# Kernel tuning notes

Measured on AMD Instinct MI355X. Metric: run time of the kernel, lower is better.

## Reference

```python
import jax, jax.numpy as jnp
import numpy as np

B = 16384          # batch_size
NF = 50            # n_fields
K = 16             # embedding_dim
V = 1_000_000      # input_dim (vocab)
H = 400            # fc hidden
NNZ = B * NF


def _xavier(key, shape):
    fan_in, fan_out = shape
    lim = (6.0 / (fan_in + fan_out)) ** 0.5
    return jax.random.uniform(key, shape, minval=-lim, maxval=lim, dtype=jnp.float32)


def setup_inputs() -> dict:
    key = jax.random.key(0)
    ks = jax.random.split(key, 12)
    feats = jax.random.randint(ks[0], (NNZ,), 0, V)
    # n_fields contiguous features per sample (required by view(batch_size,-1))
    index = jnp.repeat(jnp.arange(B), NF)
    values = jax.random.uniform(ks[1], (NNZ,), dtype=jnp.float32)
    bias = jnp.zeros((1, 1), jnp.float32)
    weights = _xavier(ks[2], (V, 1))
    embedding = _xavier(ks[3], (V, K))
    d = NF * K  # 800
    W0 = _xavier(ks[4], (d, H))
    b0 = jax.random.normal(ks[5], (1, 1), jnp.float32)
    W1 = _xavier(ks[6], (H, H))
    b1 = jax.random.normal(ks[7], (1, 1), jnp.float32)
    W2 = _xavier(ks[8], (H, 1))
    b2 = jax.random.normal(ks[9], (1, 1), jnp.float32)
    return dict(index=index, feats=feats, values=values, bias=bias,
                weights=weights, embedding=embedding,
                W0=W0, b0=b0, W1=W1, b1=b1, W2=W2, b2=b2, batch_size=B)


def reference(index, feats, values, bias, weights, embedding,
              W0, b0, W1, b1, W2, b2, batch_size):
    # gather (F.embedding)
    w = weights[feats, 0]              # [nnz]
    emb = embedding[feats]             # [nnz, K]

    # first order: segment-sum of w*v, plus bias ([B] + [1,1] -> [1,B], as in torch)
    first = jax.ops.segment_sum(w * values, index, num_segments=batch_size) + bias

    # second order: FM pooling trick, fused over all K dims in one segment reduce
    ev = emb * values[:, None]                                        # [nnz, K]
    s1 = jax.ops.segment_sum(ev, index, num_segments=batch_size)      # [B, K]
    s2 = jax.ops.segment_sum(ev * ev, index, num_segments=batch_size) # [B, K]
    second = 0.5 * jnp.sum(s1 * s1 - s2, axis=1)                      # [B]

    # higher order MLP (relu on every layer, scalar biases)
    x = emb.reshape(batch_size, -1)    # [B, NF*K]
    x = jax.nn.relu(x @ W0 + b0)
    x = jax.nn.relu(x @ W1 + b1)
    x = jax.nn.relu(x @ W2 + b2)       # [B, 1]
    higher = x.reshape(-1)             # [B]

    return jax.nn.sigmoid(first + second + higher)  # [1, B]
```

## Files before the change

### kernel.cpp

```cpp
#include <hip/hip_runtime.h>
#include <hip/hip_bf16.h>


#define BATCH 16384
#define NFLD  50
#define EK    16
#define DDIM  800
#define HDIM  400
#define HPAD  416
#define NPAD  512

#define TB_W0 400
#define TB_W1 208
#define TBLK  (TB_W0 + TB_W1)
#define GBLK  (BATCH / 16)

#define MROWS 64
#define NCOLS 448
#define P1    (DDIM / 32)
#define P2    (HPAD / 32)
#define H0S   424

#define PH1B(b) ((b) * 32768)
#define PH2B(b) ((b) * 28672)
#define H0OFF   98304
#define REDOFF  152576
#define LDSSZ   154624

#define VMCNT(N) asm volatile("s_waitcnt vmcnt(" #N ")" ::: "memory")

typedef __attribute__((ext_vector_type(8))) __bf16 bf16x8;
typedef __attribute__((ext_vector_type(4))) float  f32x4;

typedef const __attribute__((address_space(1))) unsigned int* gas_u32p;
typedef __attribute__((address_space(3))) unsigned int*       las_u32p;

__device__ __forceinline__ void gld_lds16(const void* g, void* l) {
    __builtin_amdgcn_global_load_lds((gas_u32p)g, (las_u32p)l, 16, 0, 0);
}

__device__ __forceinline__ void bar() {
    __builtin_amdgcn_sched_barrier(0);
    __builtin_amdgcn_s_barrier();
    __builtin_amdgcn_sched_barrier(0);
}

__global__ __launch_bounds__(256) void prep_kernel(
    const float* __restrict__ W0, const float* __restrict__ W1,
    __hip_bfloat16* __restrict__ W0t, __hip_bfloat16* __restrict__ W1t,
    const int* __restrict__ feats, const float* __restrict__ values,
    const float* __restrict__ biasp, const float* __restrict__ weights,
    const float* __restrict__ embedding,
    float* __restrict__ fs, __hip_bfloat16* __restrict__ x)
{
    const int bid = blockIdx.x;
    if (bid < TBLK) {
        const int which = bid >= TB_W0;
        const int i  = which ? bid - TB_W0 : bid;
        const int nx = which ? 13 : 25;
        const int bx = i % nx, by = i / nx;
        const float* src = which ? W1 : W0;
        __hip_bfloat16* dst = which ? W1t : W0t;
        const int srcK = which ? HDIM : DDIM;
        const int dstCols = which ? HPAD : DDIM;

        __shared__ float tile[32][33];
        const int tx = threadIdx.x & 31, ty = threadIdx.x >> 5;
        const int k0 = bx * 32, n0 = by * 32;
#pragma unroll
        for (int r = 0; r < 4; ++r) {
            int k = k0 + ty + r * 8;
            int n = n0 + tx;
            float v = (k < srcK && n < HDIM) ? src[(long)k * HDIM + n] : 0.f;
            tile[ty + r * 8][tx] = v;
        }
        __syncthreads();
#pragma unroll
        for (int r = 0; r < 4; ++r) {
            int n = n0 + ty + r * 8;
            int k = k0 + tx;
            if (k < dstCols)
                dst[(long)n * dstCols + k] = __float2bfloat16(tile[tx][ty + r * 8]);
        }
        return;
    }

    const int wave = threadIdx.x >> 6;
    const int lane = threadIdx.x & 63;
    const int r    = lane >> 2, c = lane & 3;
    const int sbase = (bid - TBLK) * 16 + wave * 4;

    int   f[4] = {0, 0, 0, 0};
    float v[4] = {0.f, 0.f, 0.f, 0.f};
    float wsum[4] = {0.f, 0.f, 0.f, 0.f};
#pragma unroll
    for (int q = 0; q < 4; ++q) {
        const long base = (long)(sbase + q) * NFLD;
        if (lane < NFLD) {
            f[q] = feats[base + lane];
            v[q] = values[base + lane];
            wsum[q] = weights[f[q]] * v[q];
        }
    }

    int   fj[4][4]; float vj[4][4];
#pragma unroll
    for (int q = 0; q < 4; ++q)
#pragma unroll
        for (int p = 0; p < 4; ++p) {
            const int j = p * 16 + r;
            if (p < 3 || r < 2) {
                fj[q][p] = __shfl(f[q], j);
                vj[q][p] = __shfl(v[q], j);
            }
        }
    float4 e[4][4];
#pragma unroll
    for (int q = 0; q < 4; ++q)
#pragma unroll
        for (int p = 0; p < 4; ++p)
            if (p < 3 || r < 2)
                e[q][p] = *(const float4*)(embedding + (long)fj[q][p] * EK + c * 4);

#pragma unroll
    for (int q = 0; q < 4; ++q) {
        const int s = sbase + q;
        f32x4 s1 = {0.f, 0.f, 0.f, 0.f}, s2 = {0.f, 0.f, 0.f, 0.f};
#pragma unroll
        for (int p = 0; p < 4; ++p) {
            const int j = p * 16 + r;
            if (p < 3 || r < 2) {
                f32x4 ef = {e[q][p].x, e[q][p].y, e[q][p].z, e[q][p].w};
                f32x4 ev = ef * vj[q][p];
                s1 += ev;
                s2 += ev * ev;
                __hip_bfloat16 pk[4] = {
                    __float2bfloat16(e[q][p].x), __float2bfloat16(e[q][p].y),
                    __float2bfloat16(e[q][p].z), __float2bfloat16(e[q][p].w)};
                *(uint2*)&x[(long)s * DDIM + j * EK + c * 4] = *(uint2*)pk;
            }
        }
#pragma unroll
        for (int m = 4; m <= 32; m <<= 1) {
            s1.x += __shfl_xor(s1.x, m); s1.y += __shfl_xor(s1.y, m);
            s1.z += __shfl_xor(s1.z, m); s1.w += __shfl_xor(s1.w, m);
            s2.x += __shfl_xor(s2.x, m); s2.y += __shfl_xor(s2.y, m);
            s2.z += __shfl_xor(s2.z, m); s2.w += __shfl_xor(s2.w, m);
        }
        float t = (s1.x * s1.x - s2.x) + (s1.y * s1.y - s2.y)
                + (s1.z * s1.z - s2.z) + (s1.w * s1.w - s2.w);
        t += __shfl_xor(t, 1); t += __shfl_xor(t, 2);
        float w = wsum[q];
        w += __shfl_xor(w, 1);  w += __shfl_xor(w, 2);
        w += __shfl_xor(w, 4);  w += __shfl_xor(w, 8);
        w += __shfl_xor(w, 16); w += __shfl_xor(w, 32);
        if (lane == 0) fs[s] = w + 0.5f * t + biasp[0];
    }
}

__global__ __launch_bounds__(448) void fused_mlp_kernel(
    const __hip_bfloat16* __restrict__ x,
    const __hip_bfloat16* __restrict__ W0t, const __hip_bfloat16* __restrict__ W1t,
    const float* __restrict__ b0p, const float* __restrict__ b1p,
    const float* __restrict__ W2, const float* __restrict__ b2p,
    const float* __restrict__ fs, float* __restrict__ out)
{
    __shared__ __align__(16) char lds[LDSSZ];
    __hip_bfloat16* h0p = (__hip_bfloat16*)(lds + H0OFF);
    float*          red = (float*)(lds + REDOFF);

    const int tid  = threadIdx.x;
    const int wave = tid >> 6, lane = tid & 63;
    const int l16  = lane & 15, quad = lane >> 4;
    const int m0 = blockIdx.x * MROWS;
    const int nbase = wave * 64;

    const int rl  = lane >> 2;
    const int swc = ((lane & 3) ^ ((lane >> 3) & 3)) * 8;
    const int qsw = (quad ^ ((l16 >> 1) & 3)) * 8;

    const float b0 = b0p[0];
    const float b1 = b1p[0];

    const int sstart = (wave < 4) ? wave * 5 : 20 + (wave - 4) * 4;
    const int scnt   = (wave < 4) ? 5 : 4;
    auto stage1 = [&](int p, int b) {
        const int k0 = p * 32;
        char* dst = lds + PH1B(b);
#pragma unroll
        for (int c = 0; c < 5; ++c) {
            if (c < scnt) {
                const int id = sstart + c;
                const __hip_bfloat16* src = (id < 4)
                    ? x   + (long)(m0 + id * 16 + rl) * DDIM + k0 + swc
                    : W0t + (long)((id - 4) * 16 + rl) * DDIM + k0 + swc;
                gld_lds16(src, dst + id * 1024 + lane * 16);
            }
        }
    };

    f32x4 acc[4][4] = {};
    auto compute1 = [&](int b) {
        const __hip_bfloat16* s = (const __hip_bfloat16*)(lds + PH1B(b));
        bf16x8 af[4], bfr[4];
#pragma unroll
        for (int i = 0; i < 4; ++i)
            af[i] = *(const bf16x8*)&s[i * 512 + l16 * 32 + qsw];
#pragma unroll
        for (int j = 0; j < 4; ++j)
            bfr[j] = *(const bf16x8*)&s[(4 + wave * 4 + j) * 512 + l16 * 32 + qsw];
        __builtin_amdgcn_s_setprio(1);
#pragma unroll
        for (int i = 0; i < 4; ++i)
#pragma unroll
            for (int j = 0; j < 4; ++j)
                acc[i][j] = __builtin_amdgcn_mfma_f32_16x16x32_bf16(
                    af[i], bfr[j], acc[i][j], 0, 0, 0);
        __builtin_amdgcn_s_setprio(0);
    };

    stage1(0, 0);
    stage1(1, 1);
    for (int p = 0; p < P1; ++p) {
        if (p + 1 < P1) { VMCNT(4); } else { VMCNT(0); }
        bar();
        if (p + 2 < P1) stage1(p + 2, (p + 2) % 3);
        compute1(p % 3);
    }
    bar();

    auto stage2 = [&](int p, int b) {
        const int k0 = p * 32;
#pragma unroll
        for (int c = 0; c < 4; ++c) {
            const int ch = wave * 4 + c;
            gld_lds16(W1t + (long)(ch * 16 + rl) * HPAD + k0 + swc,
                      lds + PH2B(b) + ch * 1024 + lane * 16);
        }
    };
    stage2(0, 0);
    stage2(1, 1);

#pragma unroll
    for (int i = 0; i < 4; ++i)
#pragma unroll
        for (int j = 0; j < 4; ++j) {
            const int col = nbase + j * 16 + l16;
            if (col < HPAD) {
#pragma unroll
                for (int r = 0; r < 4; ++r) {
                    const int row = i * 16 + quad * 4 + r;
                    float v = acc[i][j][r] + b0;
                    v = v > 0.f ? v : 0.f;
                    if (col >= HDIM) v = 0.f;
                    h0p[row * H0S + col] = __float2bfloat16(v);
                }
            }
        }

    f32x4 acc2[4][4] = {};
    float w2v[4];
#pragma unroll
    for (int j = 0; j < 4; ++j) {
        const int col = nbase + j * 16 + l16;
        w2v[j] = (col < HDIM) ? W2[col] : 0.f;
    }
    auto compute2 = [&](int p, int b) {
        const __hip_bfloat16* s = (const __hip_bfloat16*)(lds + PH2B(b));
        bf16x8 af[4], bfr[4];
#pragma unroll
        for (int i = 0; i < 4; ++i)
            af[i] = *(const bf16x8*)&h0p[(i * 16 + l16) * H0S + p * 32 + quad * 8];
#pragma unroll
        for (int j = 0; j < 4; ++j)
            bfr[j] = *(const bf16x8*)&s[(wave * 4 + j) * 512 + l16 * 32 + qsw];
        __builtin_amdgcn_s_setprio(1);
#pragma unroll
        for (int i = 0; i < 4; ++i)
#pragma unroll
            for (int j = 0; j < 4; ++j)
                acc2[i][j] = __builtin_amdgcn_mfma_f32_16x16x32_bf16(
                    af[i], bfr[j], acc2[i][j], 0, 0, 0);
        __builtin_amdgcn_s_setprio(0);
    };

    asm volatile("s_waitcnt lgkmcnt(0)" ::: "memory");
    bar();

    for (int p = 0; p < P2; ++p) {
        if (p + 1 < P2) { VMCNT(4); } else { VMCNT(0); }
        bar();
        if (p + 2 < P2) stage2(p + 2, (p + 2) % 3);
        compute2(p, p % 3);
    }

    if (tid < MROWS) red[tid * 8 + 7] = 0.f;
#pragma unroll
    for (int i = 0; i < 4; ++i)
#pragma unroll
        for (int r = 0; r < 4; ++r) {
            float ps = 0.f;
#pragma unroll
            for (int j = 0; j < 4; ++j) {
                float v = acc2[i][j][r] + b1;
                v = v > 0.f ? v : 0.f;
                ps += v * w2v[j];
            }
            ps += __shfl_xor(ps, 1); ps += __shfl_xor(ps, 2);
            ps += __shfl_xor(ps, 4); ps += __shfl_xor(ps, 8);
            if (l16 == 0)
                red[(i * 16 + quad * 4 + r) * 8 + wave] = ps;
        }
    __syncthreads();

    if (tid < MROWS) {
        const float4 r0 = *(const float4*)&red[tid * 8];
        const float4 r1 = *(const float4*)&red[tid * 8 + 4];
        const float s = ((r0.x + r0.y) + (r0.z + r0.w))
                      + ((r1.x + r1.y) + (r1.z + r1.w));
        float hv = s + b2p[0];
        hv = hv > 0.f ? hv : 0.f;
        const float z = fs[m0 + tid] + hv;
        out[m0 + tid] = 1.f / (1.f + __expf(-z));
    }
}

extern "C" void kernel_launch(void* const* d_in, const int* in_sizes, int n_in,
                              void* d_out, int out_size, void* d_ws, size_t ws_size,
                              hipStream_t stream)
{
    const int*   feats     = (const int*)d_in[1];
    const float* values    = (const float*)d_in[2];
    const float* bias      = (const float*)d_in[3];
    const float* weights   = (const float*)d_in[4];
    const float* embedding = (const float*)d_in[5];
    const float* W0 = (const float*)d_in[6];
    const float* b0 = (const float*)d_in[7];
    const float* W1 = (const float*)d_in[8];
    const float* b1 = (const float*)d_in[9];
    const float* W2 = (const float*)d_in[10];
    const float* b2 = (const float*)d_in[11];

    char* ws = (char*)d_ws;
    size_t off = 0;
    auto alloc = [&](size_t bytes) {
        void* p = ws + off;
        off += (bytes + 255) & ~(size_t)255;
        return p;
    };
    float*          fs   = (float*)alloc((size_t)BATCH * 4);
    __hip_bfloat16* x    = (__hip_bfloat16*)alloc((size_t)BATCH * DDIM * 2);
    __hip_bfloat16* W0t  = (__hip_bfloat16*)alloc((size_t)NPAD * DDIM * 2);
    __hip_bfloat16* W1t  = (__hip_bfloat16*)alloc((size_t)NPAD * HPAD * 2);
    (void)ws_size; (void)in_sizes; (void)n_in; (void)out_size;

    prep_kernel<<<dim3(TBLK + GBLK), 256, 0, stream>>>(
        W0, W1, W0t, W1t, feats, values, bias, weights, embedding, fs, x);
    fused_mlp_kernel<<<dim3(BATCH / MROWS), 448, 0, stream>>>(
        x, W0t, W1t, b0, b1, W2, b2, fs, (float*)d_out);
}
```

Baseline: 167.5 us.

## Fuse embedding gather and FM pooling into the MLP kernel via LDS

The embedding gather, first/second-order FM sums and bf16 packing of the activation panel move from the prep kernel into the fused MLP kernel. Each block gathers its 64 rows directly into a swizzled LDS panel, so the bf16 x matrix and the fs vector no longer round-trip through global memory. The block grows to 512 threads with only 7 waves doing MFMA, and W0/W1 staging drops from triple to double buffering with full vmcnt(0) waits. The risks are a serialized gather latency at kernel start and less load/compute overlap in the GEMM loops.

Measured after the change: 173.0 us. +3.3%, slower.

```diff
diff --git a/kernel.cpp b/kernel.cpp
--- a/kernel.cpp
+++ b/kernel.cpp
@@ -13,19 +13,17 @@
 #define TB_W0 400
 #define TB_W1 208
 #define TBLK  (TB_W0 + TB_W1)
-#define GBLK  (BATCH / 16)
 
 #define MROWS 64
-#define NCOLS 448
 #define P1    (DDIM / 32)
 #define P2    (HPAD / 32)
 #define H0S   424
 
-#define PH1B(b) ((b) * 32768)
-#define PH2B(b) ((b) * 28672)
-#define H0OFF   98304
-#define REDOFF  152576
-#define LDSSZ   154624
+#define BOFF   102400
+#define BBUF   28672
+#define REDOFF (BOFF + 2 * BBUF)
+#define FSLOFF (REDOFF + 2048)
+#define LDSSZ  (FSLOFF + 256)
 
 #define VMCNT(N) asm volatile("s_waitcnt vmcnt(" #N ")" ::: "memory")
 
@@ -47,168 +45,141 @@
 
 __global__ __launch_bounds__(256) void prep_kernel(
     const float* __restrict__ W0, const float* __restrict__ W1,
-    __hip_bfloat16* __restrict__ W0t, __hip_bfloat16* __restrict__ W1t,
+    __hip_bfloat16* __restrict__ W0t, __hip_bfloat16* __restrict__ W1t)
+{
+    const int bid = blockIdx.x;
+    const int which = bid >= TB_W0;
+    const int i  = which ? bid - TB_W0 : bid;
+    const int nx = which ? 13 : 25;
+    const int bx = i % nx, by = i / nx;
+    const float* src = which ? W1 : W0;
+    __hip_bfloat16* dst = which ? W1t : W0t;
+    const int srcK = which ? HDIM : DDIM;
+    const int dstCols = which ? HPAD : DDIM;
+
+    __shared__ float tile[32][33];
+    const int tx = threadIdx.x & 31, ty = threadIdx.x >> 5;
+    const int k0 = bx * 32, n0 = by * 32;
+#pragma unroll
+    for (int r = 0; r < 4; ++r) {
+        int k = k0 + ty + r * 8;
+        int n = n0 + tx;
+        float v = (k < srcK && n < HDIM) ? src[(long)k * HDIM + n] : 0.f;
+        tile[ty + r * 8][tx] = v;
+    }
+    __syncthreads();
+#pragma unroll
+    for (int r = 0; r < 4; ++r) {
+        int n = n0 + ty + r * 8;
+        int k = k0 + tx;
+        if (k < dstCols)
+            dst[(long)n * dstCols + k] = __float2bfloat16(tile[tx][ty + r * 8]);
+    }
+}
+
+__global__ __launch_bounds__(512, 2) void fused_mlp_kernel(
     const int* __restrict__ feats, const float* __restrict__ values,
     const float* __restrict__ biasp, const float* __restrict__ weights,
     const float* __restrict__ embedding,
-    float* __restrict__ fs, __hip_bfloat16* __restrict__ x)
-{
-    const int bid = blockIdx.x;
-    if (bid < TBLK) {
-        const int which = bid >= TB_W0;
-        const int i  = which ? bid - TB_W0 : bid;
-        const int nx = which ? 13 : 25;
-        const int bx = i % nx, by = i / nx;
-        const float* src = which ? W1 : W0;
-        __hip_bfloat16* dst = which ? W1t : W0t;
-        const int srcK = which ? HDIM : DDIM;
-        const int dstCols = which ? HPAD : DDIM;
-
-        __shared__ float tile[32][33];
-        const int tx = threadIdx.x & 31, ty = threadIdx.x >> 5;
-        const int k0 = bx * 32, n0 = by * 32;
-#pragma unroll
-        for (int r = 0; r < 4; ++r) {
-            int k = k0 + ty + r * 8;
-            int n = n0 + tx;
-            float v = (k < srcK && n < HDIM) ? src[(long)k * HDIM + n] : 0.f;
-            tile[ty + r * 8][tx] = v;
-        }
-        __syncthreads();
-#pragma unroll
-        for (int r = 0; r < 4; ++r) {
-            int n = n0 + ty + r * 8;
-            int k = k0 + tx;
-            if (k < dstCols)
-                dst[(long)n * dstCols + k] = __float2bfloat16(tile[tx][ty + r * 8]);
-        }
-        return;
-    }
-
-    const int wave = threadIdx.x >> 6;
-    const int lane = threadIdx.x & 63;
-    const int r    = lane >> 2, c = lane & 3;
-    const int sbase = (bid - TBLK) * 16 + wave * 4;
-
-    int   f[4] = {0, 0, 0, 0};
-    float v[4] = {0.f, 0.f, 0.f, 0.f};
-    float wsum[4] = {0.f, 0.f, 0.f, 0.f};
-#pragma unroll
-    for (int q = 0; q < 4; ++q) {
-        const long base = (long)(sbase + q) * NFLD;
-        if (lane < NFLD) {
-            f[q] = feats[base + lane];
-            v[q] = values[base + lane];
-            wsum[q] = weights[f[q]] * v[q];
-        }
-    }
-
-    int   fj[4][4]; float vj[4][4];
-#pragma unroll
-    for (int q = 0; q < 4; ++q)
-#pragma unroll
-        for (int p = 0; p < 4; ++p) {
-            const int j = p * 16 + r;
-            if (p < 3 || r < 2) {
-                fj[q][p] = __shfl(f[q], j);
-                vj[q][p] = __shfl(v[q], j);
-            }
-        }
-    float4 e[4][4];
-#pragma unroll
-    for (int q = 0; q < 4; ++q)
-#pragma unroll
-        for (int p = 0; p < 4; ++p)
-            if (p < 3 || r < 2)
-                e[q][p] = *(const float4*)(embedding + (long)fj[q][p] * EK + c * 4);
-
-#pragma unroll
-    for (int q = 0; q < 4; ++q) {
-        const int s = sbase + q;
-        f32x4 s1 = {0.f, 0.f, 0.f, 0.f}, s2 = {0.f, 0.f, 0.f, 0.f};
-#pragma unroll
-        for (int p = 0; p < 4; ++p) {
-            const int j = p * 16 + r;
-            if (p < 3 || r < 2) {
-                f32x4 ef = {e[q][p].x, e[q][p].y, e[q][p].z, e[q][p].w};
-                f32x4 ev = ef * vj[q][p];
-                s1 += ev;
-                s2 += ev * ev;
-                __hip_bfloat16 pk[4] = {
-                    __float2bfloat16(e[q][p].x), __float2bfloat16(e[q][p].y),
-                    __float2bfloat16(e[q][p].z), __float2bfloat16(e[q][p].w)};
-                *(uint2*)&x[(long)s * DDIM + j * EK + c * 4] = *(uint2*)pk;
-            }
-        }
-#pragma unroll
-        for (int m = 4; m <= 32; m <<= 1) {
-            s1.x += __shfl_xor(s1.x, m); s1.y += __shfl_xor(s1.y, m);
-            s1.z += __shfl_xor(s1.z, m); s1.w += __shfl_xor(s1.w, m);
-            s2.x += __shfl_xor(s2.x, m); s2.y += __shfl_xor(s2.y, m);
-            s2.z += __shfl_xor(s2.z, m); s2.w += __shfl_xor(s2.w, m);
-        }
-        float t = (s1.x * s1.x - s2.x) + (s1.y * s1.y - s2.y)
-                + (s1.z * s1.z - s2.z) + (s1.w * s1.w - s2.w);
-        t += __shfl_xor(t, 1); t += __shfl_xor(t, 2);
-        float w = wsum[q];
-        w += __shfl_xor(w, 1);  w += __shfl_xor(w, 2);
-        w += __shfl_xor(w, 4);  w += __shfl_xor(w, 8);
-        w += __shfl_xor(w, 16); w += __shfl_xor(w, 32);
-        if (lane == 0) fs[s] = w + 0.5f * t + biasp[0];
-    }
-}
-
-__global__ __launch_bounds__(448) void fused_mlp_kernel(
-    const __hip_bfloat16* __restrict__ x,
     const __hip_bfloat16* __restrict__ W0t, const __hip_bfloat16* __restrict__ W1t,
     const float* __restrict__ b0p, const float* __restrict__ b1p,
     const float* __restrict__ W2, const float* __restrict__ b2p,
-    const float* __restrict__ fs, float* __restrict__ out)
+    float* __restrict__ out)
 {
     __shared__ __align__(16) char lds[LDSSZ];
-    __hip_bfloat16* h0p = (__hip_bfloat16*)(lds + H0OFF);
+    __hip_bfloat16* h0p = (__hip_bfloat16*)lds;
     float*          red = (float*)(lds + REDOFF);
+    float*          fsl = (float*)(lds + FSLOFF);
 
     const int tid  = threadIdx.x;
     const int wave = tid >> 6, lane = tid & 63;
     const int l16  = lane & 15, quad = lane >> 4;
     const int m0 = blockIdx.x * MROWS;
-    const int nbase = wave * 64;
 
     const int rl  = lane >> 2;
     const int swc = ((lane & 3) ^ ((lane >> 3) & 3)) * 8;
     const int qsw = (quad ^ ((l16 >> 1) & 3)) * 8;
 
-    const float b0 = b0p[0];
-    const float b1 = b1p[0];
-
-    const int sstart = (wave < 4) ? wave * 5 : 20 + (wave - 4) * 4;
-    const int scnt   = (wave < 4) ? 5 : 4;
-    auto stage1 = [&](int p, int b) {
-        const int k0 = p * 32;
-        char* dst = lds + PH1B(b);
-#pragma unroll
-        for (int c = 0; c < 5; ++c) {
-            if (c < scnt) {
-                const int id = sstart + c;
-                const __hip_bfloat16* src = (id < 4)
-                    ? x   + (long)(m0 + id * 16 + rl) * DDIM + k0 + swc
-                    : W0t + (long)((id - 4) * 16 + rl) * DDIM + k0 + swc;
-                gld_lds16(src, dst + id * 1024 + lane * 16);
+    auto stageB = [&](const __hip_bfloat16* Bt, int ldb, int p, int b) {
+        const int k0  = p * 32;
+        const int nst = (wave < 4) ? 4 : 3;
+        const int st0 = (wave < 4) ? wave * 4 : 16 + (wave - 4) * 3;
+#pragma unroll
+        for (int c = 0; c < 4; ++c) {
+            if (c < nst) {
+                const int ch = st0 + c;
+                gld_lds16(Bt + (long)(ch * 16 + rl) * ldb + k0 + swc,
+                          lds + BOFF + b * BBUF + ch * 1024 + lane * 16);
             }
         }
     };
 
+    stageB(W0t, DDIM, 0, 0);
+
+    {
+        const int s   = tid >> 3;
+        const int sub = tid & 7;
+        const int cq  = sub & 3;
+        const int jh  = sub >> 2;
+        const long sb = (long)(m0 + s) * NFLD;
+        const int pr = s & 15, pg = s >> 4;
+        const int pbase = pg * 1024 + pr * 64 + (cq & 1) * 8;
+        const int sxor  = (pr >> 1) & 3;
+
+        f32x4 s1v = {0.f, 0.f, 0.f, 0.f}, s2v = {0.f, 0.f, 0.f, 0.f};
+        float wsum = 0.f;
+#pragma unroll
+        for (int g = 0; g < 5; ++g) {
+            int ff[5]; float vv[5]; float4 ee[5];
+#pragma unroll
+            for (int k = 0; k < 5; ++k) ff[k] = feats[sb + jh * 25 + g * 5 + k];
+#pragma unroll
+            for (int k = 0; k < 5; ++k) vv[k] = values[sb + jh * 25 + g * 5 + k];
+#pragma unroll
+            for (int k = 0; k < 5; ++k)
+                ee[k] = *(const float4*)(embedding + (long)ff[k] * EK + cq * 4);
+#pragma unroll
+            for (int k = 0; k < 5; ++k) {
+                const int j = jh * 25 + g * 5 + k;
+                f32x4 ef = {ee[k].x, ee[k].y, ee[k].z, ee[k].w};
+                f32x4 ev = ef * vv[k];
+                s1v += ev;
+                s2v += ev * ev;
+                if (cq == 0) wsum += weights[ff[k]] * vv[k];
+                __hip_bfloat16 pk[4] = {
+                    __float2bfloat16(ee[k].x), __float2bfloat16(ee[k].y),
+                    __float2bfloat16(ee[k].z), __float2bfloat16(ee[k].w)};
+                const int slot = (j & 1) * 2 + (cq >> 1);
+                *(uint2*)(lds + (j >> 1) * 4096 + pbase + (slot ^ sxor) * 16) =
+                    *(uint2*)pk;
+            }
+        }
+        s1v.x += __shfl_xor(s1v.x, 4); s1v.y += __shfl_xor(s1v.y, 4);
+        s1v.z += __shfl_xor(s1v.z, 4); s1v.w += __shfl_xor(s1v.w, 4);
+        s2v.x += __shfl_xor(s2v.x, 4); s2v.y += __shfl_xor(s2v.y, 4);
+        s2v.z += __shfl_xor(s2v.z, 4); s2v.w += __shfl_xor(s2v.w, 4);
+        wsum  += __shfl_xor(wsum, 4);
+        float tq = (s1v.x * s1v.x - s2v.x) + (s1v.y * s1v.y - s2v.y)
+                 + (s1v.z * s1v.z - s2v.z) + (s1v.w * s1v.w - s2v.w);
+        tq += __shfl_xor(tq, 1); tq += __shfl_xor(tq, 2);
+        if (sub == 0) fsl[s] = wsum + 0.5f * tq + biasp[0];
+    }
+    asm volatile("s_waitcnt lgkmcnt(0)" ::: "memory");
+
+    const float b0 = b0p[0];
+    const float b1 = b1p[0];
+
     f32x4 acc[4][4] = {};
-    auto compute1 = [&](int b) {
-        const __hip_bfloat16* s = (const __hip_bfloat16*)(lds + PH1B(b));
+    auto compute1 = [&](int p, int b) {
+        const __hip_bfloat16* pan = (const __hip_bfloat16*)lds;
+        const __hip_bfloat16* sB  = (const __hip_bfloat16*)(lds + BOFF + b * BBUF);
         bf16x8 af[4], bfr[4];
 #pragma unroll
         for (int i = 0; i < 4; ++i)
-            af[i] = *(const bf16x8*)&s[i * 512 + l16 * 32 + qsw];
+            af[i] = *(const bf16x8*)&pan[p * 2048 + i * 512 + l16 * 32 + qsw];
 #pragma unroll
         for (int j = 0; j < 4; ++j)
-            bfr[j] = *(const bf16x8*)&s[(4 + wave * 4 + j) * 512 + l16 * 32 + qsw];
+            bfr[j] = *(const bf16x8*)&sB[(wave * 4 + j) * 512 + l16 * 32 + qsw];
         __builtin_amdgcn_s_setprio(1);
 #pragma unroll
         for (int i = 0; i < 4; ++i)
@@ -219,61 +190,47 @@
         __builtin_amdgcn_s_setprio(0);
     };
 
-    stage1(0, 0);
-    stage1(1, 1);
     for (int p = 0; p < P1; ++p) {
-        if (p + 1 < P1) { VMCNT(4); } else { VMCNT(0); }
+        VMCNT(0);
         bar();
-        if (p + 2 < P1) stage1(p + 2, (p + 2) % 3);
-        compute1(p % 3);
+        if (p + 1 < P1) stageB(W0t, DDIM, p + 1, (p + 1) & 1);
+        if (wave < 7) compute1(p, p & 1);
     }
     bar();
 
-    auto stage2 = [&](int p, int b) {
-        const int k0 = p * 32;
-#pragma unroll
-        for (int c = 0; c < 4; ++c) {
-            const int ch = wave * 4 + c;
-            gld_lds16(W1t + (long)(ch * 16 + rl) * HPAD + k0 + swc,
-                      lds + PH2B(b) + ch * 1024 + lane * 16);
-        }
-    };
-    stage2(0, 0);
-    stage2(1, 1);
-
-#pragma unroll
-    for (int i = 0; i < 4; ++i)
-#pragma unroll
-        for (int j = 0; j < 4; ++j) {
-            const int col = nbase + j * 16 + l16;
-            if (col < HPAD) {
-#pragma unroll
-                for (int r = 0; r < 4; ++r) {
-                    const int row = i * 16 + quad * 4 + r;
-                    float v = acc[i][j][r] + b0;
-                    v = v > 0.f ? v : 0.f;
-                    if (col >= HDIM) v = 0.f;
-                    h0p[row * H0S + col] = __float2bfloat16(v);
+    stageB(W1t, HPAD, 0, 0);
+
+    if (wave < 7) {
+#pragma unroll
+        for (int i = 0; i < 4; ++i)
+#pragma unroll
+            for (int j = 0; j < 4; ++j) {
+                const int col = wave * 64 + j * 16 + l16;
+                if (col < HPAD) {
+#pragma unroll
+                    for (int r = 0; r < 4; ++r) {
+                        const int row = i * 16 + quad * 4 + r;
+                        float v = acc[i][j][r] + b0;
+                        v = v > 0.f ? v : 0.f;
+                        if (col >= HDIM) v = 0.f;
+                        h0p[row * H0S + col] = __float2bfloat16(v);
+                    }
                 }
             }
-        }
+    }
+    asm volatile("s_waitcnt lgkmcnt(0)" ::: "memory");
+    bar();
 
     f32x4 acc2[4][4] = {};
-    float w2v[4];
-#pragma unroll
-    for (int j = 0; j < 4; ++j) {
-        const int col = nbase + j * 16 + l16;
-        w2v[j] = (col < HDIM) ? W2[col] : 0.f;
-    }
     auto compute2 = [&](int p, int b) {
-        const __hip_bfloat16* s = (const __hip_bfloat16*)(lds + PH2B(b));
+        const __hip_bfloat16* sB = (const __hip_bfloat16*)(lds + BOFF + b * BBUF);
         bf16x8 af[4], bfr[4];
 #pragma unroll
         for (int i = 0; i < 4; ++i)
             af[i] = *(const bf16x8*)&h0p[(i * 16 + l16) * H0S + p * 32 + quad * 8];
 #pragma unroll
         for (int j = 0; j < 4; ++j)
-            bfr[j] = *(const bf16x8*)&s[(wave * 4 + j) * 512 + l16 * 32 + qsw];
+            bfr[j] = *(const bf16x8*)&sB[(wave * 4 + j) * 512 + l16 * 32 + qsw];
         __builtin_amdgcn_s_setprio(1);
 #pragma unroll
         for (int i = 0; i < 4; ++i)
@@ -284,43 +241,48 @@
         __builtin_amdgcn_s_setprio(0);
     };
 
-    asm volatile("s_waitcnt lgkmcnt(0)" ::: "memory");
-    bar();
-
     for (int p = 0; p < P2; ++p) {
-        if (p + 1 < P2) { VMCNT(4); } else { VMCNT(0); }
+        VMCNT(0);
         bar();
-        if (p + 2 < P2) stage2(p + 2, (p + 2) % 3);
-        compute2(p, p % 3);
+        if (p + 1 < P2) stageB(W1t, HPAD, p + 1, (p + 1) & 1);
+        if (wave < 7) compute2(p, p & 1);
     }
 
     if (tid < MROWS) red[tid * 8 + 7] = 0.f;
-#pragma unroll
-    for (int i = 0; i < 4; ++i)
-#pragma unroll
-        for (int r = 0; r < 4; ++r) {
-            float ps = 0.f;
-#pragma unroll
-            for (int j = 0; j < 4; ++j) {
-                float v = acc2[i][j][r] + b1;
-                v = v > 0.f ? v : 0.f;
-                ps += v * w2v[j];
+    if (wave < 7) {
+        float w2v[4];
+#pragma unroll
+        for (int j = 0; j < 4; ++j) {
+            const int col = wave * 64 + j * 16 + l16;
+            w2v[j] = (col < HDIM) ? W2[col] : 0.f;
+        }
+#pragma unroll
+        for (int i = 0; i < 4; ++i)
+#pragma unroll
+            for (int r = 0; r < 4; ++r) {
+                float ps = 0.f;
+#pragma unroll
+                for (int j = 0; j < 4; ++j) {
+                    float v = acc2[i][j][r] + b1;
+                    v = v > 0.f ? v : 0.f;
+                    ps += v * w2v[j];
+                }
+                ps += __shfl_xor(ps, 1); ps += __shfl_xor(ps, 2);
+                ps += __shfl_xor(ps, 4); ps += __shfl_xor(ps, 8);
+                if (l16 == 0)
+                    red[(i * 16 + quad * 4 + r) * 8 + wave] = ps;
             }
-            ps += __shfl_xor(ps, 1); ps += __shfl_xor(ps, 2);
-            ps += __shfl_xor(ps, 4); ps += __shfl_xor(ps, 8);
-            if (l16 == 0)
-                red[(i * 16 + quad * 4 + r) * 8 + wave] = ps;
-        }
+    }
     __syncthreads();
 
     if (tid < MROWS) {
         const float4 r0 = *(const float4*)&red[tid * 8];
         const float4 r1 = *(const float4*)&red[tid * 8 + 4];
-        const float s = ((r0.x + r0.y) + (r0.z + r0.w))
-                      + ((r1.x + r1.y) + (r1.z + r1.w));
-        float hv = s + b2p[0];
+        const float sm = ((r0.x + r0.y) + (r0.z + r0.w))
+                       + ((r1.x + r1.y) + (r1.z + r1.w));
+        float hv = sm + b2p[0];
         hv = hv > 0.f ? hv : 0.f;
-        const float z = fs[m0 + tid] + hv;
+        const float z = fsl[tid] + hv;
         out[m0 + tid] = 1.f / (1.f + __expf(-z));
     }
 }
@@ -348,14 +310,12 @@
         off += (bytes + 255) & ~(size_t)255;
         return p;
     };
-    float*          fs   = (float*)alloc((size_t)BATCH * 4);
-    __hip_bfloat16* x    = (__hip_bfloat16*)alloc((size_t)BATCH * DDIM * 2);
-    __hip_bfloat16* W0t  = (__hip_bfloat16*)alloc((size_t)NPAD * DDIM * 2);
-    __hip_bfloat16* W1t  = (__hip_bfloat16*)alloc((size_t)NPAD * HPAD * 2);
+    __hip_bfloat16* W0t = (__hip_bfloat16*)alloc((size_t)NPAD * DDIM * 2);
+    __hip_bfloat16* W1t = (__hip_bfloat16*)alloc((size_t)NPAD * HPAD * 2);
     (void)ws_size; (void)in_sizes; (void)n_in; (void)out_size;
 
-    prep_kernel<<<dim3(TBLK + GBLK), 256, 0, stream>>>(
-        W0, W1, W0t, W1t, feats, values, bias, weights, embedding, fs, x);
-    fused_mlp_kernel<<<dim3(BATCH / MROWS), 448, 0, stream>>>(
-        x, W0t, W1t, b0, b1, W2, b2, fs, (float*)d_out);
-}
+    prep_kernel<<<dim3(TBLK), 256, 0, stream>>>(W0, W1, W0t, W1t);
+    fused_mlp_kernel<<<dim3(BATCH / MROWS), 512, 0, stream>>>(
+        feats, values, bias, weights, embedding,
+        W0t, W1t, b0, b1, W2, b2, (float*)d_out);
+}
```
